# Kernel tuning notes

Measured on AMD Instinct MI355X. Metric: run time of the kernel, lower is better.

## Reference

```python
import jax, jax.numpy as jnp
import numpy as np

N_NODES = 50000
N_EDGES = 800000
N_GRAPHS = 1024
NODE_IN = 128
HID = 300
DEPTH = 5
READOUT = 1024


def setup_inputs() -> dict:
    key = jax.random.key(0)
    ks = jax.random.split(key, 12)
    x = jax.random.normal(ks[0], (N_NODES, NODE_IN), dtype=jnp.float32)
    edge_index = jax.random.randint(ks[1], (2, N_EDGES), 0, N_NODES, dtype=jnp.int32)
    batch = jnp.sort(jax.random.randint(ks[2], (N_NODES,), 0, N_GRAPHS, dtype=jnp.int32))
    s_in = 1.0 / np.sqrt(NODE_IN)
    s_h = 1.0 / np.sqrt(HID)
    W_proj = jax.random.normal(ks[3], (NODE_IN, HID), dtype=jnp.float32) * s_in
    b_proj = jnp.zeros((HID,), dtype=jnp.float32)
    W1 = jax.random.normal(ks[4], (DEPTH, HID, HID), dtype=jnp.float32) * s_h
    b1 = jnp.zeros((DEPTH, HID), dtype=jnp.float32)
    W2 = jax.random.normal(ks[5], (DEPTH, HID, HID), dtype=jnp.float32) * s_h
    b2 = jnp.zeros((DEPTH, HID), dtype=jnp.float32)
    W_sp = jax.random.normal(ks[6], (HID, READOUT), dtype=jnp.float32) * s_h
    b_sp = jnp.zeros((READOUT,), dtype=jnp.float32)
    prelu_a = jnp.full((1,), 0.25, dtype=jnp.float32)  # nn.PReLU default
    return {"x": x, "edge_index": edge_index, "batch": batch,
            "W_proj": W_proj, "b_proj": b_proj, "W1": W1, "b1": b1,
            "W2": W2, "b2": b2, "W_sp": W_sp, "b_sp": b_sp, "prelu_a": prelu_a}


def reference(x, edge_index, batch, W_proj, b_proj, W1, b1, W2, b2, W_sp, b_sp, prelu_a):
    # project_node_feats: Linear + ReLU
    h = jax.nn.relu(x @ W_proj + b_proj)  # [N, HID]
    src = edge_index[0]
    dst = edge_index[1]
    for i in range(DEPTH):
        # GINConv (eps=0): out = nn(x + sum_{j in N(i)} x_j)
        agg = h + jax.ops.segment_sum(h[src], dst, num_segments=N_NODES)
        h = jax.nn.relu(agg @ W1[i] + b1[i]) @ W2[i] + b2[i]
        if i < DEPTH - 1:
            h = jax.nn.relu(h)
        # dropout is identity in eval mode
    # global_add_pool over graph ids
    pooled = jax.ops.segment_sum(h, batch, num_segments=N_GRAPHS)  # [G, HID]
    z = pooled @ W_sp + b_sp  # [G, READOUT]
    # PReLU with single shared parameter
    readout = jnp.where(z >= 0, z, prelu_a[0] * z)
    return readout
```

## Files before the change

kernel.cpp:

```cpp
#include <hip/hip_runtime.h>
#include <cstdint>

#define N_NODES 50000
#define N_EDGES 800000
#define N_GRAPHS 1024
#define NODE_IN 128
#define HID 300
#define DEPTH 5
#define READOUT 1024
#define PSTR 320

typedef float f32x4 __attribute__((ext_vector_type(4)));
typedef short bf16x8 __attribute__((ext_vector_type(8)));
typedef unsigned short us8 __attribute__((ext_vector_type(8)));

__device__ inline unsigned short f2bf(float v) {
    unsigned u = __float_as_uint(v);
    unsigned r = u + 0x7FFFu + ((u >> 16) & 1u);
    return (unsigned short)(r >> 16);
}
__device__ inline float bf2f(unsigned short h) {
    return __uint_as_float((unsigned)h << 16);
}
__device__ inline float bflo(unsigned u) { return __uint_as_float(u << 16); }
__device__ inline float bfhi(unsigned u) { return __uint_as_float(u & 0xFFFF0000u); }
__device__ inline unsigned packbf(float a, float b) {
    return (unsigned)f2bf(a) | ((unsigned)f2bf(b) << 16);
}

__global__ void hist2(const int* __restrict__ dst, int* __restrict__ cnt,
                      const int* __restrict__ batch, int* __restrict__ gcnt) {
    int i = blockIdx.x * blockDim.x + threadIdx.x;
    if (i < N_EDGES) atomicAdd(&cnt[dst[i]], 1);
    else if (i < N_EDGES + N_NODES) atomicAdd(&gcnt[batch[i - N_EDGES]], 1);
}

__global__ __launch_bounds__(256)
void scan_block2(const int* __restrict__ cnt, int* __restrict__ offs, int* __restrict__ bsum,
                 const int* __restrict__ gcnt, int* __restrict__ goffs, int* __restrict__ gsum,
                 int nbn) {
    __shared__ int buf[256];
    int b = blockIdx.x;
    const int* in; int* out; int* bs; int n; int bi;
    if (b < nbn) { in = cnt; out = offs; bs = bsum; n = N_NODES; bi = b; }
    else { in = gcnt; out = goffs; bs = gsum; n = N_GRAPHS; bi = b - nbn; }
    int i = bi * 256 + (int)threadIdx.x;
    int v = (i < n) ? in[i] : 0;
    buf[threadIdx.x] = v;
    __syncthreads();
    for (int off = 1; off < 256; off <<= 1) {
        int t = ((int)threadIdx.x >= off) ? buf[threadIdx.x - off] : 0;
        __syncthreads();
        buf[threadIdx.x] += t;
        __syncthreads();
    }
    if (i < n) out[i] = buf[threadIdx.x] - v;
    if (threadIdx.x == 255) bs[bi] = buf[255];
}

__global__ __launch_bounds__(256)
void scan_base2(const int* __restrict__ bsum, int* __restrict__ bbase, int nbn, int* __restrict__ tot_n,
                const int* __restrict__ gsum, int* __restrict__ gbase, int nbg, int* __restrict__ tot_g) {
    __shared__ int buf[256];
    const int* bs; int* bb; int nb; int* tot;
    if (blockIdx.x == 0) { bs = bsum; bb = bbase; nb = nbn; tot = tot_n; }
    else { bs = gsum; bb = gbase; nb = nbg; tot = tot_g; }
    int v = ((int)threadIdx.x < nb) ? bs[threadIdx.x] : 0;
    buf[threadIdx.x] = v;
    __syncthreads();
    for (int off = 1; off < 256; off <<= 1) {
        int t = ((int)threadIdx.x >= off) ? buf[threadIdx.x - off] : 0;
        __syncthreads();
        buf[threadIdx.x] += t;
        __syncthreads();
    }
    if ((int)threadIdx.x < nb) bb[threadIdx.x] = buf[threadIdx.x] - v;
    if (threadIdx.x == 255) *tot = buf[255];
}

__global__ void scan_add2(int* __restrict__ offs, const int* __restrict__ bbase,
                          int* __restrict__ cursor,
                          int* __restrict__ goffs, const int* __restrict__ gbase, int nbn) {
    int b = blockIdx.x;
    if (b < nbn) {
        int i = b * 256 + (int)threadIdx.x;
        if (i < N_NODES) {
            int o = offs[i] + bbase[b];
            offs[i] = o;
            cursor[i] = o;
        }
    } else {
        int bi = b - nbn;
        int i = bi * 256 + (int)threadIdx.x;
        if (i < N_GRAPHS) goffs[i] += gbase[bi];
    }
}

__global__ void scatter_kernel(const int* __restrict__ src, const int* __restrict__ dst,
                               int* __restrict__ cursor, int* __restrict__ csr, int n) {
    int i = blockIdx.x * blockDim.x + threadIdx.x;
    if (i < n) {
        int p = atomicAdd(&cursor[dst[i]], 1);
        csr[p] = src[i];
    }
}

__global__ __launch_bounds__(256)
void aggregate_bf16(const unsigned short* __restrict__ h, const int* __restrict__ offs,
                    const int* __restrict__ csr, unsigned short* __restrict__ out) {
    int wave = (int)((blockIdx.x * blockDim.x + threadIdx.x) >> 6);
    int lane = threadIdx.x & 63;
    if (wave >= N_NODES) return;
    bool act = lane < 40;
    size_t lo = (size_t)lane * 8;
    float a0 = 0.f, a1 = 0.f, a2 = 0.f, a3 = 0.f, a4 = 0.f, a5 = 0.f, a6 = 0.f, a7 = 0.f;
    if (act) {
        uint4 v = *(const uint4*)(h + (size_t)wave * PSTR + lo);
        a0 = bflo(v.x); a1 = bfhi(v.x); a2 = bflo(v.y); a3 = bfhi(v.y);
        a4 = bflo(v.z); a5 = bfhi(v.z); a6 = bflo(v.w); a7 = bfhi(v.w);
    }
    int s = offs[wave], e = offs[wave + 1];
    int k = s;
    for (; k + 3 < e; k += 4) {
        int i0 = csr[k], i1 = csr[k + 1], i2 = csr[k + 2], i3 = csr[k + 3];
        if (act) {
            uint4 v0 = *(const uint4*)(h + (size_t)i0 * PSTR + lo);
            uint4 v1 = *(const uint4*)(h + (size_t)i1 * PSTR + lo);
            uint4 v2 = *(const uint4*)(h + (size_t)i2 * PSTR + lo);
            uint4 v3 = *(const uint4*)(h + (size_t)i3 * PSTR + lo);
            a0 += bflo(v0.x) + bflo(v1.x) + bflo(v2.x) + bflo(v3.x);
            a1 += bfhi(v0.x) + bfhi(v1.x) + bfhi(v2.x) + bfhi(v3.x);
            a2 += bflo(v0.y) + bflo(v1.y) + bflo(v2.y) + bflo(v3.y);
            a3 += bfhi(v0.y) + bfhi(v1.y) + bfhi(v2.y) + bfhi(v3.y);
            a4 += bflo(v0.z) + bflo(v1.z) + bflo(v2.z) + bflo(v3.z);
            a5 += bfhi(v0.z) + bfhi(v1.z) + bfhi(v2.z) + bfhi(v3.z);
            a6 += bflo(v0.w) + bflo(v1.w) + bflo(v2.w) + bflo(v3.w);
            a7 += bfhi(v0.w) + bfhi(v1.w) + bfhi(v2.w) + bfhi(v3.w);
        }
    }
    for (; k < e; ++k) {
        int i0 = csr[k];
        if (act) {
            uint4 v = *(const uint4*)(h + (size_t)i0 * PSTR + lo);
            a0 += bflo(v.x); a1 += bfhi(v.x); a2 += bflo(v.y); a3 += bfhi(v.y);
            a4 += bflo(v.z); a5 += bfhi(v.z); a6 += bflo(v.w); a7 += bfhi(v.w);
        }
    }
    if (act) {
        uint4 w;
        w.x = packbf(a0, a1); w.y = packbf(a2, a3);
        w.z = packbf(a4, a5); w.w = packbf(a6, a7);
        *(uint4*)(out + (size_t)wave * PSTR + lo) = w;
    }
}

__global__ __launch_bounds__(256)
void split_all(const float* __restrict__ W1, const float* __restrict__ W2,
               const float* __restrict__ Wsp, const float* __restrict__ Wproj,
               unsigned short* __restrict__ w1H, unsigned short* __restrict__ w2H,
               unsigned short* __restrict__ spH, unsigned short* __restrict__ spL,
               unsigned short* __restrict__ pjH, unsigned short* __restrict__ pjL) {
    __shared__ float tile[32][33];
    const int LAYER_SZ = 320 * 320;
    int z = blockIdx.z;
    const float* W; unsigned short* H = nullptr; unsigned short* L = nullptr;
    int K, N, KP;
    if (z < 10) {
        if (blockIdx.x >= 10) return;
        int l = z % 5;
        W = (z < 5 ? W1 : W2) + (size_t)l * HID * HID;
        H = (z < 5 ? w1H : w2H) + (size_t)l * LAYER_SZ;
        K = HID; N = HID; KP = 320;
    } else if (z == 10) {
        W = Wsp; H = spH; L = spL; K = HID; N = READOUT; KP = 320;
    } else {
        if (blockIdx.x >= 10 || blockIdx.y >= 4) return;
        W = Wproj; H = pjH; L = pjL; K = NODE_IN; N = HID; KP = 128;
    }
    int n0 = blockIdx.x * 32, k0 = blockIdx.y * 32;
    int tx = threadIdx.x & 31, ty = threadIdx.x >> 5;
#pragma unroll
    for (int r = 0; r < 4; ++r) {
        int k = k0 + ty + r * 8, n = n0 + tx;
        tile[ty + r * 8][tx] = (k < K && n < N) ? W[(size_t)k * N + n] : 0.f;
    }
    __syncthreads();
#pragma unroll
    for (int r = 0; r < 4; ++r) {
        int n = n0 + ty + r * 8, k = k0 + tx;
        float v = tile[tx][ty + r * 8];
        unsigned short hb = f2bf(v);
        H[(size_t)n * KP + k] = hb;
        if (L) L[(size_t)n * KP + k] = f2bf(v - bf2f(hb));
    }
}

#define BSWZ(r, c) ((c) ^ (((r) >> 1) & 3))

__global__ __launch_bounds__(512)
void gin_mlp(const unsigned short* __restrict__ Ap, int M,
             const unsigned short* __restrict__ B1, const float* __restrict__ b1,
             const unsigned short* __restrict__ B2, const float* __restrict__ b2,
             unsigned short* __restrict__ Op, int act2) {
    __shared__ __align__(16) unsigned short At[128 * 320];
    __shared__ __align__(16) unsigned short Bs[2][10240];

    const int tid = threadIdx.x;
    const int bm = blockIdx.x * 128;
    const int wid = tid >> 6, lane = tid & 63;
    const int wm = wid >> 2, wn = wid & 3;
    const int lr = lane & 15, lk = lane >> 4;

    float b1v[5], b2v[5];
#pragma unroll
    for (int n = 0; n < 5; ++n) {
        int col = wn * 80 + n * 16 + lr;
        b1v[n] = (col < HID) ? b1[col] : 0.f;
        b2v[n] = (col < HID) ? b2[col] : 0.f;
    }

    size_t bofs[3]; int bldso[3]; bool bval[3];
#pragma unroll
    for (int i = 0; i < 3; ++i) {
        int q = i * 512 + tid;
        bval[i] = q < 1280;
        int r = (q < 1280 ? q : 0) >> 2, c = q & 3;
        bofs[i] = (size_t)r * 320 + c * 8;
        bldso[i] = r * 32 + BSWZ(r, c) * 8;
    }

    us8 vB[3];
    auto LOADB = [&](const unsigned short* B, int t) {
        int k0 = t * 32;
#pragma unroll
        for (int i = 0; i < 3; ++i)
            if (bval[i]) vB[i] = *(const us8*)&B[bofs[i] + k0];
    };
    auto WRITEB = [&](int b) {
#pragma unroll
        for (int i = 0; i < 3; ++i)
            if (bval[i]) *(us8*)&Bs[b][bldso[i]] = vB[i];
    };

    LOADB(B1, 0);

#pragma unroll
    for (int i = 0; i < 10; ++i) {
        int g = i * 512 + tid;
        int row = g / 40, c = g - row * 40;
        int grow = bm + row; if (grow >= M) grow = M - 1;
        us8 v = *(const us8*)&Ap[(size_t)grow * PSTR + c * 8];
        *(us8*)&At[row * 320 + (c ^ (row & 7)) * 8] = v;
    }
    WRITEB(0);
    LOADB(B1, 1);
    __syncthreads();

    f32x4 acc[4][5];

    auto RUN = [&](const unsigned short* B, const unsigned short* Bnext) {
        for (int t = 0; t < 10; ++t) {
            bf16x8 aS[4];
#pragma unroll
            for (int m = 0; m < 4; ++m) {
                int row = wm * 64 + m * 16 + lr;
                int c = t * 4 + lk;
                aS[m] = *(const bf16x8*)&At[row * 320 + (c ^ (row & 7)) * 8];
            }
#pragma unroll
            for (int n = 0; n < 5; ++n) {
                int rb = wn * 80 + n * 16 + lr;
                bf16x8 bh = *(const bf16x8*)&Bs[t & 1][rb * 32 + BSWZ(rb, lk) * 8];
#pragma unroll
                for (int m = 0; m < 4; ++m)
                    acc[m][n] = __builtin_amdgcn_mfma_f32_16x16x32_bf16(aS[m], bh, acc[m][n], 0, 0, 0);
            }
            if (t < 9) {
                WRITEB((t + 1) & 1);
                if (t < 8) LOADB(B, t + 2);
                else if (Bnext) LOADB(Bnext, 0);
            }
            __syncthreads();
        }
    };

#pragma unroll
    for (int m = 0; m < 4; ++m)
#pragma unroll
        for (int n = 0; n < 5; ++n) acc[m][n] = (f32x4)0.f;
    RUN(B1, B2);

#pragma unroll
    for (int n = 0; n < 5; ++n) {
        int col = wn * 80 + n * 16 + lr;
        int cc = col >> 3, cp = col & 7;
        float bv = b1v[n];
        bool vc = col < HID;
#pragma unroll
        for (int m = 0; m < 4; ++m) {
#pragma unroll
            for (int p = 0; p < 4; ++p) {
                int row = wm * 64 + m * 16 + lk * 4 + p;
                float v = vc ? fmaxf(acc[m][n][p] + bv, 0.f) : 0.f;
                At[row * 320 + ((cc ^ (row & 7)) * 8) + cp] = f2bf(v);
            }
        }
    }
    WRITEB(0);
    LOADB(B2, 1);
    __syncthreads();

#pragma unroll
    for (int m = 0; m < 4; ++m)
#pragma unroll
        for (int n = 0; n < 5; ++n) acc[m][n] = (f32x4)0.f;
    RUN(B2, nullptr);

#pragma unroll
    for (int n = 0; n < 5; ++n) {
        int col = wn * 80 + n * 16 + lr;
        int cc = col >> 3, cp = col & 7;
        float bv = b2v[n];
        bool vc = col < HID;
#pragma unroll
        for (int m = 0; m < 4; ++m) {
#pragma unroll
            for (int p = 0; p < 4; ++p) {
                int row = wm * 64 + m * 16 + lk * 4 + p;
                float v = vc ? (acc[m][n][p] + bv) : 0.f;
                if (act2) v = fmaxf(v, 0.f);
                At[row * 320 + ((cc ^ (row & 7)) * 8) + cp] = f2bf(v);
            }
        }
    }
    __syncthreads();
#pragma unroll
    for (int i = 0; i < 10; ++i) {
        int g = i * 512 + tid;
        int row = g / 40, c = g - row * 40;
        int grow = bm + row;
        if (grow < M)
            *(us8*)&Op[(size_t)grow * PSTR + c * 8] =
                *(const us8*)&At[row * 320 + (c ^ (row & 7)) * 8];
    }
}

__global__ __launch_bounds__(256)
void gemm_f32A(const float* __restrict__ A, int lda, int M, int K, int KP,
               const unsigned short* __restrict__ BH, const unsigned short* __restrict__ BL, int KPB,
               const float* __restrict__ bias, int N,
               float* __restrict__ C, int ldc, unsigned short* __restrict__ Op, int outPlane,
               int act, const float* __restrict__ prelu) {
    __shared__ __align__(16) unsigned short AsH[64 * 40];
    __shared__ __align__(16) unsigned short AsL[64 * 40];
    __shared__ __align__(16) unsigned short BsH[320 * 40];
    __shared__ __align__(16) unsigned short BsL[320 * 40];

    const int tid = threadIdx.x;
    const int bm = blockIdx.y * 64;
    const int bn = blockIdx.x * 320;
    const int wid = tid >> 6, lane = tid & 63;
    const int lr = lane & 15, lk = lane >> 4;
    const int ar = tid >> 2, ac = tid & 3;

    f32x4 acc[4][5];
#pragma unroll
    for (int m = 0; m < 4; ++m)
#pragma unroll
        for (int n = 0; n < 5; ++n) acc[m][n] = (f32x4)0.f;

    for (int k0 = 0; k0 < KP; k0 += 32) {
        {
            int gm = bm + ar;
            int k = k0 + ac * 8;
            float v[8];
#pragma unroll
            for (int j = 0; j < 8; ++j) v[j] = 0.f;
            if (gm < M) {
                if (k + 7 < K) {
                    float4 p0 = *(const float4*)&A[(size_t)gm * lda + k];
                    float4 p1 = *(const float4*)&A[(size_t)gm * lda + k + 4];
                    v[0] = p0.x; v[1] = p0.y; v[2] = p0.z; v[3] = p0.w;
                    v[4] = p1.x; v[5] = p1.y; v[6] = p1.z; v[7] = p1.w;
                } else {
#pragma unroll
                    for (int j = 0; j < 8; ++j)
                        if (k + j < K) v[j] = A[(size_t)gm * lda + k + j];
                }
            }
            us8 h, l;
#pragma unroll
            for (int j = 0; j < 8; ++j) {
                unsigned short hb = f2bf(v[j]);
                h[j] = hb;
                l[j] = f2bf(v[j] - bf2f(hb));
            }
            *(us8*)&AsH[ar * 40 + ac * 8] = h;
            *(us8*)&AsL[ar * 40 + ac * 8] = l;
        }
#pragma unroll
        for (int p = 0; p < 5; ++p) {
            int r = ar + p * 64;
            size_t gb = (size_t)(bn + r) * KPB + k0 + ac * 8;
            *(us8*)&BsH[r * 40 + ac * 8] = *(const us8*)&BH[gb];
            *(us8*)&BsL[r * 40 + ac * 8] = *(const us8*)&BL[gb];
        }
        __syncthreads();
        bf16x8 aH[4], aL[4];
#pragma unroll
        for (int m = 0; m < 4; ++m) {
            aH[m] = *(const bf16x8*)&AsH[(m * 16 + lr) * 40 + lk * 8];
            aL[m] = *(const bf16x8*)&AsL[(m * 16 + lr) * 40 + lk * 8];
        }
#pragma unroll
        for (int n = 0; n < 5; ++n) {
            int r = wid * 80 + n * 16 + lr;
            bf16x8 bh = *(const bf16x8*)&BsH[r * 40 + lk * 8];
            bf16x8 bl = *(const bf16x8*)&BsL[r * 40 + lk * 8];
#pragma unroll
            for (int m = 0; m < 4; ++m) {
                acc[m][n] = __builtin_amdgcn_mfma_f32_16x16x32_bf16(aH[m], bh, acc[m][n], 0, 0, 0);
                acc[m][n] = __builtin_amdgcn_mfma_f32_16x16x32_bf16(aH[m], bl, acc[m][n], 0, 0, 0);
                acc[m][n] = __builtin_amdgcn_mfma_f32_16x16x32_bf16(aL[m], bh, acc[m][n], 0, 0, 0);
            }
        }
        __syncthreads();
    }
    float slope = (act == 2) ? prelu[0] : 0.f;
#pragma unroll
    for (int n = 0; n < 5; ++n) {
        int col = bn + wid * 80 + n * 16 + lr;
        bool vc = col < N;
        float bv = vc ? bias[col] : 0.f;
#pragma unroll
        for (int m = 0; m < 4; ++m) {
            int rbase = bm + m * 16 + lk * 4;
#pragma unroll
            for (int p = 0; p < 4; ++p) {
                int row = rbase + p;
                if (row >= M) continue;
                float v = vc ? (acc[m][n][p] + bv) : 0.f;
                if (act == 1) v = fmaxf(v, 0.f);
                else if (act == 2) v = (v >= 0.f) ? v : slope * v;
                if (outPlane) {
                    if (col < PSTR) Op[(size_t)row * PSTR + col] = f2bf(v);
                } else if (vc) {
                    C[(size_t)row * ldc + col] = v;
                }
            }
        }
    }
}

__global__ __launch_bounds__(128)
void pool_seg(const unsigned short* __restrict__ h, const int* __restrict__ goffs,
              float* __restrict__ pooled) {
    __shared__ float red[6 * 64];
    int g = blockIdx.x;
    int w = threadIdx.x >> 6, lane = threadIdx.x & 63;
    int s = goffs[g], e = goffs[g + 1];
    float a0 = 0.f, a1 = 0.f, a2 = 0.f, a3 = 0.f, a4 = 0.f, a5 = 0.f;
    for (int node = s + w; node < e; node += 2) {
        const unsigned* r = (const unsigned*)(h + (size_t)node * PSTR);
        uint2 u = *(const uint2*)&r[2 * lane];
        unsigned t = (lane < 32) ? r[128 + lane] : 0u;
        a0 += bflo(u.x); a1 += bfhi(u.x);
        a2 += bflo(u.y); a3 += bfhi(u.y);
        a4 += bflo(t);   a5 += bfhi(t);
    }
    if (w == 1) {
        red[lane] = a0;        red[64 + lane] = a1;
        red[128 + lane] = a2;  red[192 + lane] = a3;
        red[256 + lane] = a4;  red[320 + lane] = a5;
    }
    __syncthreads();
    if (w == 0) {
        a0 += red[lane];        a1 += red[64 + lane];
        a2 += red[128 + lane];  a3 += red[192 + lane];
        a4 += red[256 + lane];  a5 += red[320 + lane];
        float* pr = pooled + (size_t)g * PSTR;
        *(float4*)&pr[4 * lane] = make_float4(a0, a1, a2, a3);
        if (lane < 32) *(float2*)&pr[256 + 2 * lane] = make_float2(a4, a5);
    }
}

extern "C" void kernel_launch(void* const* d_in, const int* in_sizes, int n_in,
                              void* d_out, int out_size, void* d_ws, size_t ws_size,
                              hipStream_t stream) {
    const float* x      = (const float*)d_in[0];
    const int*   eidx   = (const int*)d_in[1];
    const int*   batch  = (const int*)d_in[2];
    const float* W_proj = (const float*)d_in[3];
    const float* b_proj = (const float*)d_in[4];
    const float* W1     = (const float*)d_in[5];
    const float* b1     = (const float*)d_in[6];
    const float* W2     = (const float*)d_in[7];
    const float* b2     = (const float*)d_in[8];
    const float* W_sp   = (const float*)d_in[9];
    const float* b_sp   = (const float*)d_in[10];
    const float* prelu  = (const float*)d_in[11];

    const int* src = eidx;
    const int* dst = eidx + N_EDGES;

    const size_t PLANE = (size_t)N_NODES * PSTR + 64;
    const int LAYER_SZ = 320 * 320;
    const int SP_SZ  = 1280 * 320;
    const int PJ_SZ  = 320 * 128;
    const int NB  = (N_NODES + 255) / 256;
    const int NBG = (N_GRAPHS + 255) / 256;

    unsigned short* hA  = (unsigned short*)d_ws;
    unsigned short* hB  = hA + PLANE;
    float* pooled = (float*)(hB + PLANE);
    unsigned short* w1H = (unsigned short*)(pooled + (size_t)N_GRAPHS * PSTR + 16);
    unsigned short* w2H = w1H + 5 * (size_t)LAYER_SZ;
    unsigned short* spH = w2H + 5 * (size_t)LAYER_SZ;
    unsigned short* spL = spH + SP_SZ;
    unsigned short* pjH = spL + SP_SZ;
    unsigned short* pjL = pjH + PJ_SZ;
    int* cnt    = (int*)(((uintptr_t)(pjL + PJ_SZ) + 15) & ~(uintptr_t)15);
    int* gcnt   = cnt + N_NODES;
    int* bsum   = gcnt + N_GRAPHS;
    int* bbase  = bsum + 256;
    int* gsum   = bbase + 256;
    int* gbase  = gsum + 256;
    int* offs   = gbase + 256;
    int* goffs  = offs + N_NODES + 1;
    int* cursor = goffs + N_GRAPHS + 1;
    int* csr    = cursor + N_NODES;
    size_t needed = (size_t)((uintptr_t)(csr + N_EDGES) - (uintptr_t)d_ws);
    if (ws_size < needed) return;

    split_all<<<dim3(40, 10, 12), 256, 0, stream>>>(W1, W2, W_sp, W_proj,
                                                    w1H, w2H, spH, spL, pjH, pjL);

    hipMemsetAsync(cnt, 0, (N_NODES + N_GRAPHS) * sizeof(int), stream);
    hist2<<<(N_EDGES + N_NODES + 255) / 256, 256, 0, stream>>>(dst, cnt, batch, gcnt);
    scan_block2<<<NB + NBG, 256, 0, stream>>>(cnt, offs, bsum, gcnt, goffs, gsum, NB);
    scan_base2<<<2, 256, 0, stream>>>(bsum, bbase, NB, offs + N_NODES,
                                      gsum, gbase, NBG, goffs + N_GRAPHS);
    scan_add2<<<NB + NBG, 256, 0, stream>>>(offs, bbase, cursor, goffs, gbase, NB);
    scatter_kernel<<<(N_EDGES + 255) / 256, 256, 0, stream>>>(src, dst, cursor, csr, N_EDGES);

    gemm_f32A<<<dim3(1, (N_NODES + 63) / 64), 256, 0, stream>>>(
        x, NODE_IN, N_NODES, NODE_IN, 128, pjH, pjL, 128,
        b_proj, HID, nullptr, 0, hA, 1, 1, nullptr);

    const int GBM = (N_NODES + 127) / 128;
    unsigned short* cur = hA;
    unsigned short* agp = hB;
    for (int i = 0; i < DEPTH; ++i) {
        aggregate_bf16<<<(N_NODES * 64 + 255) / 256, 256, 0, stream>>>(cur, offs, csr, agp);
        gin_mlp<<<GBM, 512, 0, stream>>>(
            agp, N_NODES,
            w1H + (size_t)i * LAYER_SZ, b1 + (size_t)i * HID,
            w2H + (size_t)i * LAYER_SZ, b2 + (size_t)i * HID,
            cur, (i < DEPTH - 1) ? 1 : 0);
    }

    pool_seg<<<N_GRAPHS, 128, 0, stream>>>(cur, goffs, pooled);

    gemm_f32A<<<dim3(4, (N_GRAPHS + 63) / 64), 256, 0, stream>>>(
        pooled, PSTR, N_GRAPHS, HID, 320, spH, spL, 320,
        b_sp, READOUT, (float*)d_out, READOUT, nullptr, 0, 2, prelu);
}
```

Measured before the change: 860.0 us.

## Slice feature columns across blocks in GIN neighbor aggregation for cache locality

Replaces the one-wave-per-node aggregation with a sliced scheme. Each block handles one of 8 column slices of 40 bf16 features for 24 nodes, with 10 lanes per node each loading 4 features. Blocks are interleaved so that consecutive blocks cover different slices of the same node group. The aim is to shrink the gathered working set per slice so it fits better in L2/MALL and to cut idle lanes (24 of 64 lanes were idle before). In exchange the CSR indices are read 8 times, loads are narrower (8-byte instead of 16-byte), and 4 of 64 lanes per wave stay idle.

```diff
diff --git a/kernel.cpp b/kernel.cpp
--- a/kernel.cpp
+++ b/kernel.cpp
@@ -105,53 +105,40 @@
     }
 }
 
+#define NPB 24
 __global__ __launch_bounds__(256)
-void aggregate_bf16(const unsigned short* __restrict__ h, const int* __restrict__ offs,
-                    const int* __restrict__ csr, unsigned short* __restrict__ out) {
-    int wave = (int)((blockIdx.x * blockDim.x + threadIdx.x) >> 6);
-    int lane = threadIdx.x & 63;
-    if (wave >= N_NODES) return;
-    bool act = lane < 40;
-    size_t lo = (size_t)lane * 8;
-    float a0 = 0.f, a1 = 0.f, a2 = 0.f, a3 = 0.f, a4 = 0.f, a5 = 0.f, a6 = 0.f, a7 = 0.f;
-    if (act) {
-        uint4 v = *(const uint4*)(h + (size_t)wave * PSTR + lo);
-        a0 = bflo(v.x); a1 = bfhi(v.x); a2 = bflo(v.y); a3 = bfhi(v.y);
-        a4 = bflo(v.z); a5 = bfhi(v.z); a6 = bflo(v.w); a7 = bfhi(v.w);
-    }
-    int s = offs[wave], e = offs[wave + 1];
+void aggregate_sliced(const unsigned short* __restrict__ h, const int* __restrict__ offs,
+                      const int* __restrict__ csr, unsigned short* __restrict__ out) {
+    int slice = blockIdx.x & 7;
+    int nb = blockIdx.x >> 3;
+    int wave = threadIdx.x >> 6, lane = threadIdx.x & 63;
+    int g = lane / 10, e = lane - g * 10;
+    if (g >= 6) return;
+    int node = nb * NPB + wave * 6 + g;
+    if (node >= N_NODES) return;
+    size_t co = (size_t)slice * 40 + e * 4;
+    uint2 v = *(const uint2*)(h + (size_t)node * PSTR + co);
+    float a0 = bflo(v.x), a1 = bfhi(v.x), a2 = bflo(v.y), a3 = bfhi(v.y);
+    int s = offs[node], en = offs[node + 1];
     int k = s;
-    for (; k + 3 < e; k += 4) {
+    for (; k + 3 < en; k += 4) {
         int i0 = csr[k], i1 = csr[k + 1], i2 = csr[k + 2], i3 = csr[k + 3];
-        if (act) {
-            uint4 v0 = *(const uint4*)(h + (size_t)i0 * PSTR + lo);
-            uint4 v1 = *(const uint4*)(h + (size_t)i1 * PSTR + lo);
-            uint4 v2 = *(const uint4*)(h + (size_t)i2 * PSTR + lo);
-            uint4 v3 = *(const uint4*)(h + (size_t)i3 * PSTR + lo);
-            a0 += bflo(v0.x) + bflo(v1.x) + bflo(v2.x) + bflo(v3.x);
-            a1 += bfhi(v0.x) + bfhi(v1.x) + bfhi(v2.x) + bfhi(v3.x);
-            a2 += bflo(v0.y) + bflo(v1.y) + bflo(v2.y) + bflo(v3.y);
-            a3 += bfhi(v0.y) + bfhi(v1.y) + bfhi(v2.y) + bfhi(v3.y);
-            a4 += bflo(v0.z) + bflo(v1.z) + bflo(v2.z) + bflo(v3.z);
-            a5 += bfhi(v0.z) + bfhi(v1.z) + bfhi(v2.z) + bfhi(v3.z);
-            a6 += bflo(v0.w) + bflo(v1.w) + bflo(v2.w) + bflo(v3.w);
-            a7 += bfhi(v0.w) + bfhi(v1.w) + bfhi(v2.w) + bfhi(v3.w);
-        }
-    }
-    for (; k < e; ++k) {
-        int i0 = csr[k];
-        if (act) {
-            uint4 v = *(const uint4*)(h + (size_t)i0 * PSTR + lo);
-            a0 += bflo(v.x); a1 += bfhi(v.x); a2 += bflo(v.y); a3 += bfhi(v.y);
-            a4 += bflo(v.z); a5 += bfhi(v.z); a6 += bflo(v.w); a7 += bfhi(v.w);
-        }
-    }
-    if (act) {
-        uint4 w;
-        w.x = packbf(a0, a1); w.y = packbf(a2, a3);
-        w.z = packbf(a4, a5); w.w = packbf(a6, a7);
-        *(uint4*)(out + (size_t)wave * PSTR + lo) = w;
-    }
+        uint2 v0 = *(const uint2*)(h + (size_t)i0 * PSTR + co);
+        uint2 v1 = *(const uint2*)(h + (size_t)i1 * PSTR + co);
+        uint2 v2 = *(const uint2*)(h + (size_t)i2 * PSTR + co);
+        uint2 v3 = *(const uint2*)(h + (size_t)i3 * PSTR + co);
+        a0 += bflo(v0.x) + bflo(v1.x) + bflo(v2.x) + bflo(v3.x);
+        a1 += bfhi(v0.x) + bfhi(v1.x) + bfhi(v2.x) + bfhi(v3.x);
+        a2 += bflo(v0.y) + bflo(v1.y) + bflo(v2.y) + bflo(v3.y);
+        a3 += bfhi(v0.y) + bfhi(v1.y) + bfhi(v2.y) + bfhi(v3.y);
+    }
+    for (; k < en; ++k) {
+        uint2 vv = *(const uint2*)(h + (size_t)csr[k] * PSTR + co);
+        a0 += bflo(vv.x); a1 += bfhi(vv.x);
+        a2 += bflo(vv.y); a3 += bfhi(vv.y);
+    }
+    uint2 w; w.x = packbf(a0, a1); w.y = packbf(a2, a3);
+    *(uint2*)(out + (size_t)node * PSTR + co) = w;
 }
 
 __global__ __launch_bounds__(256)
@@ -547,11 +534,12 @@
         x, NODE_IN, N_NODES, NODE_IN, 128, pjH, pjL, 128,
         b_proj, HID, nullptr, 0, hA, 1, 1, nullptr);
 
-    const int GBM = (N_NODES + 127) / 128;
+    const int GBM  = (N_NODES + 127) / 128;
+    const int GAGG = ((N_NODES + NPB - 1) / NPB) * 8;
     unsigned short* cur = hA;
     unsigned short* agp = hB;
     for (int i = 0; i < DEPTH; ++i) {
-        aggregate_bf16<<<(N_NODES * 64 + 255) / 256, 256, 0, stream>>>(cur, offs, csr, agp);
+        aggregate_sliced<<<GAGG, 256, 0, stream>>>(cur, offs, csr, agp);
         gin_mlp<<<GBM, 512, 0, stream>>>(
             agp, N_NODES,
             w1H + (size_t)i * LAYER_SZ, b1 + (size_t)i * HID,
```

Result: slower. 1.194 ms (+38.9%).
